# Kernel optimization log

Hardware: AMD Instinct MI355X
Metric: run time of the kernel (lower is better)

Reference implementation:

```python
import jax, jax.numpy as jnp
import numpy as np

N = 80000       # nodes
E = 1280000     # edges (avg degree 16)
G = 2000        # graphs
NSHAPE, NCOLOR, POSMAX = 16, 16, 1024
HID, OUT, IN_DIM = 64, 2, 40
EPS = 1e-5


def setup_inputs() -> dict:
    key = jax.random.key(0)
    ks = jax.random.split(key, 20)
    f32 = jnp.float32
    return {
        "shape_id": jax.random.randint(ks[0], (N,), 0, NSHAPE),
        "color_id": jax.random.randint(ks[1], (N,), 0, NCOLOR),
        "pos_id": jax.random.randint(ks[2], (N,), 0, POSMAX),
        "edge_index": jax.random.randint(ks[3], (2, E), 0, N),
        "batch": jnp.sort(jax.random.randint(ks[4], (N,), 0, G)),
        "num_graphs": G,
        "shape_tab": jax.random.normal(ks[5], (NSHAPE, 16), f32),
        "color_tab": jax.random.normal(ks[6], (NCOLOR, 16), f32),
        "pos_tab": jax.random.normal(ks[7], (POSMAX, 8), f32),
        "W1l": jax.random.normal(ks[8], (IN_DIM, HID), f32) / np.sqrt(IN_DIM),
        "b1": jnp.zeros((HID,), f32),
        "W1r": jax.random.normal(ks[9], (IN_DIM, HID), f32) / np.sqrt(IN_DIM),
        "g1": jnp.ones((HID,), f32),
        "be1": jnp.zeros((HID,), f32),
        "W2l": jax.random.normal(ks[10], (HID, HID), f32) / np.sqrt(HID),
        "b2": jnp.zeros((HID,), f32),
        "W2r": jax.random.normal(ks[11], (HID, HID), f32) / np.sqrt(HID),
        "g2": jnp.ones((HID,), f32),
        "be2": jnp.zeros((HID,), f32),
        "Wout": jax.random.normal(ks[12], (HID, OUT), f32) / np.sqrt(HID),
        "bout": jnp.zeros((OUT,), f32),
    }


def sage_conv(x, src, dst, Wl, b, Wr, n_nodes):
    # PyG SAGEConv (mean aggr): out = lin_l(mean_{j in N(i)} x_j) + lin_r(x_i)
    agg = jax.ops.segment_sum(x[src], dst, num_segments=n_nodes)     # [N, F]
    deg = jax.ops.segment_sum(jnp.ones((src.shape[0], 1), x.dtype), dst,
                              num_segments=n_nodes)                  # [N, 1]
    agg = agg / jnp.maximum(deg, 1.0)
    return agg @ Wl + b + x @ Wr


def batch_norm(x, gamma, beta):
    # training-mode BatchNorm1d over nodes
    m = x.mean(axis=0)
    v = x.var(axis=0)
    return (x - m) * (gamma / jnp.sqrt(v + EPS)) + beta


def reference(shape_id, color_id, pos_id, edge_index, batch, num_graphs,
              shape_tab, color_tab, pos_tab,
              W1l, b1, W1r, g1, be1,
              W2l, b2, W2r, g2, be2,
              Wout, bout):
    n_nodes = shape_id.shape[0]
    src, dst = edge_index[0], edge_index[1]
    x = jnp.concatenate([shape_tab[shape_id], color_tab[color_id],
                         pos_tab[pos_id]], axis=-1)                  # [N, 40]
    x = jax.nn.relu(batch_norm(sage_conv(x, src, dst, W1l, b1, W1r, n_nodes), g1, be1))
    # dropout: eval mode -> identity
    x = jax.nn.relu(batch_norm(sage_conv(x, src, dst, W2l, b2, W2r, n_nodes), g2, be2))
    # global mean pool over batch segments
    summed = jax.ops.segment_sum(x, batch, num_segments=num_graphs)   # [G, H]
    counts = jax.ops.segment_sum(jnp.ones((n_nodes, 1), x.dtype), batch,
                                 num_segments=num_graphs)
    pooled = summed / jnp.maximum(counts, 1.0)
    return pooled @ Wout + bout                                       # [G, 2]
```

## Files before the change

kernel.cpp:

```cpp
#include <hip/hip_runtime.h>

#define NN 80000
#define NE 1280000
#define NG 2000
#define HID 64
#define FIN1 40
#define BSZ 128
#define NBUK (NN / BSZ)
#define EB 8192
#define NBB ((NE + EB - 1) / EB)
#define NBBP 160
constexpr float EPS = 1e-5f;

typedef _Float16 f16;
typedef f16 f16x8 __attribute__((ext_vector_type(8)));
typedef float f32x4 __attribute__((ext_vector_type(4)));

__global__ void setup2(const int* __restrict__ sid, const int* __restrict__ cid,
                       const int* __restrict__ pid, const int* __restrict__ batch,
                       const float* __restrict__ stab, const float* __restrict__ ctab,
                       const float* __restrict__ ptab,
                       const float* __restrict__ W1l, const float* __restrict__ W1r,
                       const float* __restrict__ W2l, const float* __restrict__ W2r,
                       const int* __restrict__ dst,
                       int* __restrict__ ids, f16* __restrict__ Bt1, f16* __restrict__ Bt2,
                       int* __restrict__ gstart,
                       f16* __restrict__ stab16, f16* __restrict__ ctab16,
                       f16* __restrict__ ptab16,
                       float* __restrict__ stats,
                       int* __restrict__ bhistT, int* __restrict__ bcnt) {
    __shared__ int lh[NBUK];
    int bid = blockIdx.x;
    int tid = threadIdx.x;
    if (bid < 313) {
        int n = bid * 256 + tid;
        if (n < NN) ids[n] = sid[n] | (cid[n] << 4) | (pid[n] << 8);
    } else if (bid < 373) {
        int i = (bid - 313) * 256 + tid;
        if (i < 64 * 104) {
            int j = i / 104, k = i - j * 104;
            float v = 0.f;
            if (k < 40) v = W1l[k * 64 + j];
            else if (k < 80) v = W1r[(k - 40) * 64 + j];
            Bt1[i] = (f16)v;
        }
        int i2 = i - 64 * 104;
        if (i2 >= 0 && i2 < 64 * 136) {
            int j = i2 / 136, k = i2 - j * 136;
            float v = 0.f;
            if (k < 64) v = W2l[k * 64 + j];
            else if (k < 128) v = W2r[(k - 64) * 64 + j];
            Bt2[i2] = (f16)v;
        }
    } else if (bid < 686) {
        int n = (bid - 373) * 256 + tid;
        if (n >= NN) return;
        int cur = batch[n];
        int prev = (n == 0) ? -1 : batch[n - 1];
        for (int g = prev + 1; g <= cur; g++) gstart[g] = n;
        if (n == NN - 1)
            for (int g = cur + 1; g <= NG; g++) gstart[g] = NN;
    } else if (bid < 720) {
        int i = (bid - 686) * 256 + tid;
        if (i < 256) stab16[i] = (f16)stab[i];
        else if (i < 512) ctab16[i - 256] = (f16)ctab[i - 256];
        else if (i < 512 + 8192) ptab16[i - 512] = (f16)ptab[i - 512];
    } else if (bid == 720) {
        if (tid < 256) stats[tid] = 0.f;
    } else {
        int kb = bid - 721;
        for (int i = tid; i < NBUK; i += 256) lh[i] = 0;
        __syncthreads();
        int e0 = kb * EB, e1 = min(e0 + EB, NE);
        for (int e = e0 + tid; e < e1; e += 256) atomicAdd(&lh[dst[e] >> 7], 1);
        __syncthreads();
        for (int i = tid; i < NBUK; i += 256) {
            int c = lh[i];
            bhistT[i * NBBP + kb] = c;
            if (c) atomicAdd(&bcnt[i], c);
        }
    }
}

__global__ void kscan(const int* __restrict__ bcnt, const int* __restrict__ bhistT,
                      int* __restrict__ bstart, int* __restrict__ lbaseT) {
    int b = blockIdx.x;
    int l = threadIdx.x;
    int s = 0;
    for (int i = l; i < b; i += 64) s += bcnt[i];
#pragma unroll
    for (int off = 1; off < 64; off <<= 1) s += __shfl_xor(s, off);
    if (l == 0) bstart[b] = s;
    if (b == 0 && l == 0) bstart[NBUK] = NE;
    int run = s;
    for (int i0 = 0; i0 < NBB; i0 += 64) {
        int idx = i0 + l;
        int v = (idx < NBB) ? bhistT[b * NBBP + idx] : 0;
        int inc = v;
#pragma unroll
        for (int off = 1; off < 64; off <<= 1) {
            int tt = __shfl_up(inc, off);
            if (l >= off) inc += tt;
        }
        if (idx < NBB) lbaseT[b * NBBP + idx] = run + inc - v;
        run += __shfl(inc, 63);
    }
}

__global__ void kbin(const int* __restrict__ src, const int* __restrict__ dst,
                     const int* __restrict__ lbaseT, int* __restrict__ ebuf) {
    __shared__ int lcur[NBUK];
    for (int i = threadIdx.x; i < NBUK; i += 256) lcur[i] = lbaseT[i * NBBP + blockIdx.x];
    __syncthreads();
    int e0 = blockIdx.x * EB, e1 = min(e0 + EB, NE);
    for (int e = e0 + threadIdx.x; e < e1; e += 256) {
        int d = dst[e];
        int off = atomicAdd(&lcur[d >> 7], 1);
        ebuf[off] = (src[e] << 7) | (d & 127);
    }
}

__global__ void kfill(const int* __restrict__ ebuf, const int* __restrict__ bstart,
                      int* __restrict__ row_ptr, int* __restrict__ eidx) {
    __shared__ int cnt[BSZ];
    __shared__ int sb[BSZ];
    __shared__ int lcur[BSZ];
    int b = blockIdx.x, t = threadIdx.x;
    int nbase = b << 7;
    if (t < BSZ) cnt[t] = 0;
    __syncthreads();
    int s0 = bstart[b], s1 = bstart[b + 1];
    for (int i = s0 + t; i < s1; i += 256) atomicAdd(&cnt[ebuf[i] & 127], 1);
    __syncthreads();
    if (t < BSZ) sb[t] = cnt[t];
    __syncthreads();
    for (int off = 1; off < BSZ; off <<= 1) {
        int v = (t >= off && t < BSZ) ? sb[t - off] : 0;
        __syncthreads();
        if (t < BSZ) sb[t] += v;
        __syncthreads();
    }
    if (t < BSZ) {
        int excl = ((t == 0) ? 0 : sb[t - 1]) + s0;
        row_ptr[nbase + t] = excl;
        lcur[t] = excl;
    }
    if (b == 0 && t == 0) row_ptr[NN] = NE;
    __syncthreads();
    for (int i = s0 + t; i < s1; i += 256) {
        int v = ebuf[i];
        int pos = atomicAdd(&lcur[v & 127], 1);
        eidx[pos] = v >> 7;
    }
}

__global__ void gather1(const int* __restrict__ row_ptr, const int* __restrict__ eidx,
                        const int* __restrict__ ids,
                        const f16* __restrict__ stab16, const f16* __restrict__ ctab16,
                        const f16* __restrict__ ptab16, f16* __restrict__ agg) {
    int tt = blockIdx.x * 256 + threadIdx.x;
    int n = tt >> 6;
    int lane = threadIdx.x & 63;
    if (n >= NN) return;
    int grp = lane >> 3, li = lane & 7;
    bool act = li < 5;
    int beg = row_ptr[n], end = row_ptr[n + 1];
    f16x8 ach;
#pragma unroll
    for (int i = 0; i < 8; i++) ach[i] = (f16)0.f;
    for (int j0 = beg; j0 < end; j0 += 64) {
        int cnt = min(64, end - j0);
        int myid = (j0 + lane < end) ? eidx[j0 + lane] : 0;
        int steps = (cnt + 7) >> 3;
        for (int u = 0; u < steps; u++) {
            int e = u * 8 + grp;
            int s = __shfl(myid, e);
            if (e < cnt && act) {
                int id = ids[s];
                const f16* rowp;
                if (li < 2)      rowp = &stab16[(id & 15) * 16 + li * 8];
                else if (li < 4) rowp = &ctab16[((id >> 4) & 15) * 16 + (li - 2) * 8];
                else             rowp = &ptab16[(id >> 8) * 8];
                ach += *(const f16x8*)rowp;
            }
        }
    }
    float ac[8];
#pragma unroll
    for (int i = 0; i < 8; i++) ac[i] = (float)ach[i];
#pragma unroll
    for (int m = 8; m <= 32; m <<= 1) {
#pragma unroll
        for (int i = 0; i < 8; i++) ac[i] += __shfl_xor(ac[i], m);
    }
    if (lane < 5) {
        float inv = 1.0f / (float)max(end - beg, 1);
        f16x8 o;
#pragma unroll
        for (int i = 0; i < 8; i++) o[i] = (f16)(ac[i] * inv);
        *(f16x8*)&agg[(size_t)n * FIN1 + lane * 8] = o;
    }
}

__global__ void bn_apply16(f16* __restrict__ h, const float* __restrict__ stats,
                           const float* __restrict__ g, const float* __restrict__ be) {
    __shared__ float ssc[64], ssh[64];
    int tid = threadIdx.x;
    if (tid < 64) {
        const float invn = 1.0f / (float)NN;
        float m = stats[tid] * invn;
        float var = stats[64 + tid] * invn - m * m;
        float sc = g[tid] * __frsqrt_rn(var + EPS);
        ssc[tid] = sc;
        ssh[tid] = be[tid] - m * sc;
    }
    __syncthreads();
    int idx = blockIdx.x * 256 + tid;
    if (idx >= NN * 8) return;
    int f = (idx & 7) * 8;
    f16x8 v = *(f16x8*)&h[(size_t)idx * 8];
    f16x8 o;
#pragma unroll
    for (int i = 0; i < 8; i++) {
        float xv = (float)v[i];
        o[i] = (f16)fmaxf(fmaf(xv, ssc[f + i], ssh[f + i]), 0.f);
    }
    *(f16x8*)&h[(size_t)idx * 8] = o;
}

__global__ void gather2(const int* __restrict__ row_ptr, const int* __restrict__ eidx,
                        const f16* __restrict__ x, f16* __restrict__ agg) {
    int tt = blockIdx.x * 256 + threadIdx.x;
    int n = tt >> 6;
    int lane = threadIdx.x & 63;
    if (n >= NN) return;
    int grp = lane >> 3;
    int fl = (lane & 7) * 8;
    int beg = row_ptr[n], end = row_ptr[n + 1];
    f16x8 ach;
#pragma unroll
    for (int i = 0; i < 8; i++) ach[i] = (f16)0.f;
    for (int j0 = beg; j0 < end; j0 += 64) {
        int cnt = min(64, end - j0);
        int myid = (j0 + lane < end) ? eidx[j0 + lane] : 0;
        int steps = (cnt + 7) >> 3;
        for (int u = 0; u < steps; u++) {
            int e = u * 8 + grp;
            int s = __shfl(myid, e);
            if (e < cnt) {
                ach += *(const f16x8*)&x[(size_t)s * HID + fl];
            }
        }
    }
    float ac[8];
#pragma unroll
    for (int i = 0; i < 8; i++) ac[i] = (float)ach[i];
#pragma unroll
    for (int m = 8; m <= 32; m <<= 1) {
#pragma unroll
        for (int i = 0; i < 8; i++) ac[i] += __shfl_xor(ac[i], m);
    }
    if (lane < 8) {
        float inv = 1.0f / (float)max(end - beg, 1);
        f16x8 o;
#pragma unroll
        for (int i = 0; i < 8; i++) o[i] = (f16)(ac[i] * inv);
        *(f16x8*)&agg[(size_t)n * HID + fl] = o;
    }
}

__launch_bounds__(256)
__global__ void sage_mfma1(const int* __restrict__ ids, const f16* __restrict__ aggv,
                           const f16* __restrict__ stab16, const f16* __restrict__ ctab16,
                           const f16* __restrict__ ptab16,
                           const f16* __restrict__ Btg, const float* __restrict__ bias,
                           f16* __restrict__ h, float* __restrict__ stats) {
    __shared__ float sred[4][64];
    __shared__ float qred[4][64];
    const int KP = 104;

    int tid = threadIdx.x;
    int n0 = blockIdx.x * 64;
    int w = tid >> 6, l = tid & 63;
    int jloc = l & 15, kg = l >> 4;
    int n = n0 + w * 16 + jloc;

    f16x8 af[3];
#pragma unroll
    for (int kk = 0; kk < 3; kk++) {
        int c = kk * 4 + kg;
        if (c < 5) {
            af[kk] = *(const f16x8*)&aggv[(size_t)n * FIN1 + c * 8];
        } else if (c < 10) {
            int id = ids[n];
            int cc = c - 5;
            const f16* rowp;
            if (cc < 2)      rowp = &stab16[(id & 15) * 16 + cc * 8];
            else if (cc < 4) rowp = &ctab16[((id >> 4) & 15) * 16 + (cc - 2) * 8];
            else             rowp = &ptab16[(id >> 8) * 8];
            af[kk] = *(const f16x8*)rowp;
        } else {
#pragma unroll
            for (int i = 0; i < 8; i++) af[kk][i] = (f16)0.f;
        }
    }

    f32x4 acc[4];
#pragma unroll
    for (int jt = 0; jt < 4; jt++) {
        float bj = bias[jt * 16 + jloc];
        acc[jt] = (f32x4){bj, bj, bj, bj};
    }
#pragma unroll
    for (int kk = 0; kk < 3; kk++) {
#pragma unroll
        for (int jt = 0; jt < 4; jt++) {
            f16x8 bf = *(const f16x8*)&Btg[(jt * 16 + jloc) * KP + kk * 32 + kg * 8];
            acc[jt] = __builtin_amdgcn_mfma_f32_16x16x32_f16(af[kk], bf, acc[jt], 0, 0, 0);
        }
    }
#pragma unroll
    for (int jt = 0; jt < 4; jt++) {
        float sv = 0.f, qv = 0.f;
#pragma unroll
        for (int reg = 0; reg < 4; reg++) {
            f16 hv = (f16)acc[jt][reg];
            int nn2 = n0 + w * 16 + kg * 4 + reg;
            h[(size_t)nn2 * HID + jt * 16 + jloc] = hv;
            float v = (float)hv;
            sv += v; qv += v * v;
        }
        sv += __shfl_xor(sv, 16); sv += __shfl_xor(sv, 32);
        qv += __shfl_xor(qv, 16); qv += __shfl_xor(qv, 32);
        if (kg == 0) { sred[w][jt * 16 + jloc] = sv; qred[w][jt * 16 + jloc] = qv; }
    }
    __syncthreads();
    if (tid < 128) {
        int f2 = tid & 63, which = tid >> 6;
        float r = which ? (qred[0][f2] + qred[1][f2] + qred[2][f2] + qred[3][f2])
                        : (sred[0][f2] + sred[1][f2] + sred[2][f2] + sred[3][f2]);
        atomicAdd(&stats[which * 64 + f2], r);
    }
}

__launch_bounds__(256)
__global__ void sage_mfma2(const f16* __restrict__ x, const f16* __restrict__ aggv,
                           const f16* __restrict__ Btg, const float* __restrict__ bias,
                           f16* __restrict__ h, float* __restrict__ stats) {
    __shared__ float sred[4][64];
    __shared__ float qred[4][64];
    const int KP = 136;

    int tid = threadIdx.x;
    int n0 = blockIdx.x * 64;
    int w = tid >> 6, l = tid & 63;
    int jloc = l & 15, kg = l >> 4;
    int n = n0 + w * 16 + jloc;

    f16x8 af[4];
#pragma unroll
    for (int kk = 0; kk < 4; kk++) {
        int c = kk * 4 + kg;
        if (c < 8) af[kk] = *(const f16x8*)&aggv[(size_t)n * HID + c * 8];
        else       af[kk] = *(const f16x8*)&x[(size_t)n * HID + (c - 8) * 8];
    }

    f32x4 acc[4];
#pragma unroll
    for (int jt = 0; jt < 4; jt++) {
        float bj = bias[jt * 16 + jloc];
        acc[jt] = (f32x4){bj, bj, bj, bj};
    }
#pragma unroll
    for (int kk = 0; kk < 4; kk++) {
#pragma unroll
        for (int jt = 0; jt < 4; jt++) {
            f16x8 bf = *(const f16x8*)&Btg[(jt * 16 + jloc) * KP + kk * 32 + kg * 8];
            acc[jt] = __builtin_amdgcn_mfma_f32_16x16x32_f16(af[kk], bf, acc[jt], 0, 0, 0);
        }
    }
#pragma unroll
    for (int jt = 0; jt < 4; jt++) {
        float sv = 0.f, qv = 0.f;
#pragma unroll
        for (int reg = 0; reg < 4; reg++) {
            f16 hv = (f16)acc[jt][reg];
            int nn2 = n0 + w * 16 + kg * 4 + reg;
            h[(size_t)nn2 * HID + jt * 16 + jloc] = hv;
            float v = (float)hv;
            sv += v; qv += v * v;
        }
        sv += __shfl_xor(sv, 16); sv += __shfl_xor(sv, 32);
        qv += __shfl_xor(qv, 16); qv += __shfl_xor(qv, 32);
        if (kg == 0) { sred[w][jt * 16 + jloc] = sv; qred[w][jt * 16 + jloc] = qv; }
    }
    __syncthreads();
    if (tid < 128) {
        int f2 = tid & 63, which = tid >> 6;
        float r = which ? (qred[0][f2] + qred[1][f2] + qred[2][f2] + qred[3][f2])
                        : (sred[0][f2] + sred[1][f2] + sred[2][f2] + sred[3][f2]);
        atomicAdd(&stats[which * 64 + f2], r);
    }
}

__global__ void pool_out(const f16* __restrict__ h, const float* __restrict__ stats2,
                         const float* __restrict__ g2, const float* __restrict__ be2,
                         const int* __restrict__ gstart,
                         const float* __restrict__ Wout, const float* __restrict__ bout,
                         float* __restrict__ out) {
    __shared__ float red[4][64];
    int w = blockIdx.x;
    int tid = threadIdx.x;
    int f = tid & 63, seg = tid >> 6;
    const float invn = 1.0f / (float)NN;
    float m = stats2[f] * invn;
    float var = stats2[64 + f] * invn - m * m;
    float sc = g2[f] / sqrtf(var + EPS);
    float sh = be2[f] - m * sc;
    int n0 = gstart[w], n1 = gstart[w + 1];
    float acc = 0.f;
    for (int n = n0 + seg; n < n1; n += 4) {
        float v = fmaf((float)h[(size_t)n * HID + f], sc, sh);
        acc += fmaxf(v, 0.0f);
    }
    red[seg][f] = acc;
    __syncthreads();
    if (seg == 0) {
        acc = red[0][f] + red[1][f] + red[2][f] + red[3][f];
        float inv = 1.0f / (float)max(n1 - n0, 1);
        float p = acc * inv;
        float a0 = p * Wout[f * 2 + 0];
        float a1 = p * Wout[f * 2 + 1];
#pragma unroll
        for (int mm = 1; mm < 64; mm <<= 1) {
            a0 += __shfl_xor(a0, mm);
            a1 += __shfl_xor(a1, mm);
        }
        if (f == 0) {
            out[w * 2 + 0] = a0 + bout[0];
            out[w * 2 + 1] = a1 + bout[1];
        }
    }
}

extern "C" void kernel_launch(void* const* d_in, const int* in_sizes, int n_in,
                              void* d_out, int out_size, void* d_ws, size_t ws_size,
                              hipStream_t stream) {
    const int* sid = (const int*)d_in[0];
    const int* cid = (const int*)d_in[1];
    const int* pid = (const int*)d_in[2];
    const int* ei = (const int*)d_in[3];
    const int* batch = (const int*)d_in[4];
    const float* stab = (const float*)d_in[6];
    const float* ctab = (const float*)d_in[7];
    const float* ptab = (const float*)d_in[8];
    const float* W1l = (const float*)d_in[9];
    const float* b1 = (const float*)d_in[10];
    const float* W1r = (const float*)d_in[11];
    const float* g1 = (const float*)d_in[12];
    const float* be1 = (const float*)d_in[13];
    const float* W2l = (const float*)d_in[14];
    const float* b2 = (const float*)d_in[15];
    const float* W2r = (const float*)d_in[16];
    const float* g2 = (const float*)d_in[17];
    const float* be2 = (const float*)d_in[18];
    const float* Wout = (const float*)d_in[19];
    const float* bout = (const float*)d_in[20];

    const int* src = ei;
    const int* dst = ei + NE;

    char* p = (char*)d_ws;
    f16* agg = (f16*)p;        p += (size_t)NN * HID * 2;
    f16* h1 = (f16*)p;         p += (size_t)NN * HID * 2;
    f16* h2 = (f16*)p;         p += (size_t)NN * HID * 2;
    f16* bt1 = (f16*)p;        p += 64 * 104 * 2;
    f16* bt2 = (f16*)p;        p += 64 * 136 * 2;
    f16* stab16 = (f16*)p;     p += 256 * 2;
    f16* ctab16 = (f16*)p;     p += 256 * 2;
    f16* ptab16 = (f16*)p;     p += 8192 * 2;
    float* stats = (float*)p;  p += 256 * 4;
    int* bcnt = (int*)p;       p += NBUK * 4;
    int* ids = (int*)p;        p += (size_t)NN * 4;
    int* row_ptr = (int*)p;    p += (NN + 1) * 4;
    int* gstart = (int*)p;     p += (NG + 1) * 4;
    int* bstart = (int*)p;     p += (NBUK + 1) * 4;
    int* bhistT = (int*)p;     p += (size_t)NBUK * NBBP * 4;
    int* lbaseT = (int*)p;     p += (size_t)NBUK * NBBP * 4;
    int* ebuf = (int*)p;       p += (size_t)NE * 4;
    int* eidx = (int*)p;       p += (size_t)NE * 4;

    const int B = 256;

    hipMemsetAsync(bcnt, 0, NBUK * sizeof(int), stream);

    setup2<<<721 + NBB, B, 0, stream>>>(sid, cid, pid, batch, stab, ctab, ptab,
                                        W1l, W1r, W2l, W2r, dst,
                                        ids, bt1, bt2, gstart, stab16, ctab16, ptab16,
                                        stats, bhistT, bcnt);

    kscan<<<NBUK, 64, 0, stream>>>(bcnt, bhistT, bstart, lbaseT);
    kbin<<<NBB, B, 0, stream>>>(src, dst, lbaseT, ebuf);
    kfill<<<NBUK, B, 0, stream>>>(ebuf, bstart, row_ptr, eidx);

    gather1<<<(NN * 64 + B - 1) / B, B, 0, stream>>>(row_ptr, eidx, ids,
                                                     stab16, ctab16, ptab16, agg);
    sage_mfma1<<<NN / 64, B, 0, stream>>>(ids, agg, stab16, ctab16, ptab16,
                                          bt1, b1, h1, stats);
    bn_apply16<<<(NN * 8 + B - 1) / B, B, 0, stream>>>(h1, stats, g1, be1);

    gather2<<<(NN * 64 + B - 1) / B, B, 0, stream>>>(row_ptr, eidx, h1, agg);
    sage_mfma2<<<NN / 64, B, 0, stream>>>(h1, agg, bt2, b2, h2, stats + 128);

    pool_out<<<NG, B, 0, stream>>>(h2, stats + 128, g2, be2, gstart,
                                   Wout, bout, (float*)d_out);
}
```

Baseline: 215.5 us.

## Fold bucket scan into binning and fill kernels, drop scan kernel and memset

Removes the separate kscan kernel, the bcnt global atomics and the memset. Each kbin block now recomputes bucket totals and its own prefix offsets by reading the whole per-block histogram, and each kfill block recomputes its bucket start by summing all preceding rows. This cuts two launches and their dependencies, but adds a lot of redundant reading of the histogram: roughly 625x157 ints per kbin block, and an O(b) row sum per kfill block.

```diff
diff --git a/kernel.cpp b/kernel.cpp
--- a/kernel.cpp
+++ b/kernel.cpp
@@ -28,7 +28,7 @@
                        f16* __restrict__ stab16, f16* __restrict__ ctab16,
                        f16* __restrict__ ptab16,
                        float* __restrict__ stats,
-                       int* __restrict__ bhistT, int* __restrict__ bcnt) {
+                       int* __restrict__ bhistT) {
     __shared__ int lh[NBUK];
     int bid = blockIdx.x;
     int tid = threadIdx.x;
@@ -74,62 +74,88 @@
         int e0 = kb * EB, e1 = min(e0 + EB, NE);
         for (int e = e0 + tid; e < e1; e += 256) atomicAdd(&lh[dst[e] >> 7], 1);
         __syncthreads();
-        for (int i = tid; i < NBUK; i += 256) {
-            int c = lh[i];
-            bhistT[i * NBBP + kb] = c;
-            if (c) atomicAdd(&bcnt[i], c);
-        }
-    }
-}
-
-__global__ void kscan(const int* __restrict__ bcnt, const int* __restrict__ bhistT,
-                      int* __restrict__ bstart, int* __restrict__ lbaseT) {
-    int b = blockIdx.x;
-    int l = threadIdx.x;
-    int s = 0;
-    for (int i = l; i < b; i += 64) s += bcnt[i];
-#pragma unroll
-    for (int off = 1; off < 64; off <<= 1) s += __shfl_xor(s, off);
-    if (l == 0) bstart[b] = s;
-    if (b == 0 && l == 0) bstart[NBUK] = NE;
-    int run = s;
-    for (int i0 = 0; i0 < NBB; i0 += 64) {
-        int idx = i0 + l;
-        int v = (idx < NBB) ? bhistT[b * NBBP + idx] : 0;
-        int inc = v;
-#pragma unroll
-        for (int off = 1; off < 64; off <<= 1) {
-            int tt = __shfl_up(inc, off);
-            if (l >= off) inc += tt;
-        }
-        if (idx < NBB) lbaseT[b * NBBP + idx] = run + inc - v;
-        run += __shfl(inc, 63);
+        for (int i = tid; i < NBUK; i += 256) bhistT[i * NBBP + kb] = lh[i];
     }
 }
 
 __global__ void kbin(const int* __restrict__ src, const int* __restrict__ dst,
-                     const int* __restrict__ lbaseT, int* __restrict__ ebuf) {
-    __shared__ int lcur[NBUK];
-    for (int i = threadIdx.x; i < NBUK; i += 256) lcur[i] = lbaseT[i * NBBP + blockIdx.x];
-    __syncthreads();
-    int e0 = blockIdx.x * EB, e1 = min(e0 + EB, NE);
-    for (int e = e0 + threadIdx.x; e < e1; e += 256) {
+                     const int* __restrict__ bhistT, int* __restrict__ ebuf) {
+    __shared__ int tsum[256];
+    __shared__ int sbase[NBUK];
+    int k = blockIdx.x, t = threadIdx.x;
+    int i0 = t * 3;
+    int cs[3], pf[3];
+    int local = 0;
+#pragma unroll
+    for (int u = 0; u < 3; u++) {
+        int i = i0 + u;
+        cs[u] = 0; pf[u] = 0;
+        if (i < NBUK) {
+            const int* rowp = &bhistT[i * NBBP];
+            for (int blk = 0; blk < NBB; blk++) {
+                int v = rowp[blk];
+                cs[u] += v;
+                if (blk < k) pf[u] += v;
+            }
+        }
+        local += cs[u];
+    }
+    tsum[t] = local;
+    __syncthreads();
+    for (int off = 1; off < 256; off <<= 1) {
+        int v = (t >= off) ? tsum[t - off] : 0;
+        __syncthreads();
+        tsum[t] += v;
+        __syncthreads();
+    }
+    int excl = (t == 0) ? 0 : tsum[t - 1];
+#pragma unroll
+    for (int u = 0; u < 3; u++) {
+        int i = i0 + u;
+        if (i < NBUK) {
+            sbase[i] = excl + pf[u];
+            excl += cs[u];
+        }
+    }
+    __syncthreads();
+    int e0 = k * EB, e1 = min(e0 + EB, NE);
+    for (int e = e0 + t; e < e1; e += 256) {
         int d = dst[e];
-        int off = atomicAdd(&lcur[d >> 7], 1);
+        int off = atomicAdd(&sbase[d >> 7], 1);
         ebuf[off] = (src[e] << 7) | (d & 127);
     }
 }
 
-__global__ void kfill(const int* __restrict__ ebuf, const int* __restrict__ bstart,
+__global__ void kfill(const int* __restrict__ ebuf, const int* __restrict__ bhistT,
                       int* __restrict__ row_ptr, int* __restrict__ eidx) {
+    __shared__ int redA[256];
+    __shared__ int redB[256];
     __shared__ int cnt[BSZ];
     __shared__ int sb[BSZ];
     __shared__ int lcur[BSZ];
+    __shared__ int s0s, s1s;
     int b = blockIdx.x, t = threadIdx.x;
     int nbase = b << 7;
+    int s = 0;
+    for (int i = t; i < b; i += 256) {
+        const int* rowp = &bhistT[i * NBBP];
+        int cs = 0;
+        for (int blk = 0; blk < NBB; blk++) cs += rowp[blk];
+        s += cs;
+    }
+    int cb = 0;
+    for (int blk = t; blk < NBB; blk += 256) cb += bhistT[b * NBBP + blk];
+    redA[t] = s;
+    redB[t] = cb;
+    __syncthreads();
+    for (int off = 128; off >= 1; off >>= 1) {
+        if (t < off) { redA[t] += redA[t + off]; redB[t] += redB[t + off]; }
+        __syncthreads();
+    }
+    if (t == 0) { s0s = redA[0]; s1s = redA[0] + redB[0]; }
     if (t < BSZ) cnt[t] = 0;
     __syncthreads();
-    int s0 = bstart[b], s1 = bstart[b + 1];
+    int s0 = s0s, s1 = s1s;
     for (int i = s0 + t; i < s1; i += 256) atomicAdd(&cnt[ebuf[i] & 127], 1);
     __syncthreads();
     if (t < BSZ) sb[t] = cnt[t];
@@ -480,28 +506,22 @@
     f16* ctab16 = (f16*)p;     p += 256 * 2;
     f16* ptab16 = (f16*)p;     p += 8192 * 2;
     float* stats = (float*)p;  p += 256 * 4;
-    int* bcnt = (int*)p;       p += NBUK * 4;
     int* ids = (int*)p;        p += (size_t)NN * 4;
     int* row_ptr = (int*)p;    p += (NN + 1) * 4;
     int* gstart = (int*)p;     p += (NG + 1) * 4;
-    int* bstart = (int*)p;     p += (NBUK + 1) * 4;
     int* bhistT = (int*)p;     p += (size_t)NBUK * NBBP * 4;
-    int* lbaseT = (int*)p;     p += (size_t)NBUK * NBBP * 4;
     int* ebuf = (int*)p;       p += (size_t)NE * 4;
     int* eidx = (int*)p;       p += (size_t)NE * 4;
 
     const int B = 256;
-
-    hipMemsetAsync(bcnt, 0, NBUK * sizeof(int), stream);
 
     setup2<<<721 + NBB, B, 0, stream>>>(sid, cid, pid, batch, stab, ctab, ptab,
                                         W1l, W1r, W2l, W2r, dst,
                                         ids, bt1, bt2, gstart, stab16, ctab16, ptab16,
-                                        stats, bhistT, bcnt);
-
-    kscan<<<NBUK, 64, 0, stream>>>(bcnt, bhistT, bstart, lbaseT);
-    kbin<<<NBB, B, 0, stream>>>(src, dst, lbaseT, ebuf);
-    kfill<<<NBUK, B, 0, stream>>>(ebuf, bstart, row_ptr, eidx);
+                                        stats, bhistT);
+
+    kbin<<<NBB, B, 0, stream>>>(src, dst, bhistT, ebuf);
+    kfill<<<NBUK, B, 0, stream>>>(ebuf, bhistT, row_ptr, eidx);
 
     gather1<<<(NN * 64 + B - 1) / B, B, 0, stream>>>(row_ptr, eidx, ids,
                                                      stab16, ctab16, ptab16, agg);
```

Result: slower. 246.0 us (+14.2%).
